# Kernel tuning notes

Hardware: AMD Instinct MI355X
Metric: run time of the kernel (lower is better)

## Reference

```python
import jax, jax.numpy as jnp
import numpy as np


def _shift(w):
    # max(0, -min(w)): scalar shift making w + shift non-negative
    return jnp.maximum(0.0, -jnp.min(w))


def shifted_linear(x, W, b=None):
    # F.linear with non-negative weights plus row-sum correction
    alpha = _shift(W)
    y = x @ (W + alpha).T - alpha * jnp.sum(x, axis=-1, keepdims=True)
    if b is not None:
        y = y + b
    return y


def shifted_depthwise_conv(x, w, b):
    # x: (B, D, L), w: (D, 1, K) depthwise; causal-style padding K-1, sliced to L by caller
    alpha = _shift(w)
    k = w.shape[2]
    pad = k - 1
    dn = ('NCH', 'OIH', 'NCH')
    groups = w.shape[0]
    y = jax.lax.conv_general_dilated(x, w + alpha, (1,), [(pad, pad)],
                                     dimension_numbers=dn, feature_group_count=groups)
    ones_k = jnp.ones_like(w)
    ssum = jax.lax.conv_general_dilated(x, ones_k, (1,), [(pad, pad)],
                                        dimension_numbers=dn, feature_group_count=groups)
    return y - alpha * ssum + b[None, :, None]


def setup_inputs() -> dict:
    key = jax.random.key(0)
    ks = jax.random.split(key, 10)
    d_model, d_inner, d_state, d_conv, dt_rank = 1024, 2048, 16, 4, 64
    B, L = 2, 1024
    s = 0.05
    return {
        'hidden_states': jax.random.normal(ks[0], (B, L, d_model), jnp.float32),
        'W_in': jax.random.normal(ks[1], (2 * d_inner, d_model), jnp.float32) * s,
        'conv_w': jax.random.normal(ks[2], (d_inner, 1, d_conv), jnp.float32) * 0.3,
        'conv_b': jax.random.normal(ks[3], (d_inner,), jnp.float32) * s,
        'W_x': jax.random.normal(ks[4], (dt_rank + 2 * d_state, d_inner), jnp.float32) * s,
        'W_dt': jax.random.normal(ks[5], (d_inner, dt_rank), jnp.float32) * s,
        'dt_bias': jax.random.normal(ks[6], (d_inner,), jnp.float32),
        'W_out': jax.random.normal(ks[7], (d_model, d_inner), jnp.float32) * s,
        'A_log': jax.random.normal(ks[8], (d_inner, d_state), jnp.float32) * 0.5,
        'D': jax.random.normal(ks[9], (d_inner,), jnp.float32),
    }


def reference(hidden_states, W_in, conv_w, conv_b, W_x, W_dt, dt_bias, W_out, A_log, D):
    b, l, dm = hidden_states.shape
    d_inner = conv_w.shape[0]
    d_state = A_log.shape[1]
    dt_rank = W_dt.shape[1]

    A = jnp.exp(A_log)  # (d_inner, d_state), always positive

    # in_proj over (b*l, d_model) -> (b, 2*d_inner, l)
    xz = shifted_linear(hidden_states.reshape(b * l, dm), W_in)
    xz = xz.reshape(b, l, 2 * d_inner).transpose(0, 2, 1)
    x, z = xz[:, :d_inner], xz[:, d_inner:]

    # depthwise shifted conv + SiLU activation, truncated to seqlen
    x = jax.nn.silu(shifted_depthwise_conv(x, conv_w, conv_b)[..., :l])

    # x_proj -> dt_raw, B, C
    x_dbl = shifted_linear(x.transpose(0, 2, 1).reshape(b * l, d_inner), W_x)
    dt_raw = x_dbl[:, :dt_rank]
    Bm = x_dbl[:, dt_rank:dt_rank + d_state].reshape(b, l, d_state).transpose(0, 2, 1)  # (b,n,l)
    Cm = x_dbl[:, dt_rank + d_state:].reshape(b, l, d_state).transpose(0, 2, 1)         # (b,n,l)
    dt = shifted_linear(dt_raw, W_dt).reshape(b, l, d_inner).transpose(0, 2, 1)          # (b,d,l)

    # delta activation (softplus) with bias, clamped
    delta = jnp.clip(jax.nn.softplus(dt + dt_bias[None, :, None]), 1e-4, 20.0)

    # global scalar shifts for B and C
    beta = _shift(Bm)
    gamma = _shift(Cm)
    B_nn = Bm + beta
    C_nn = Cm + gamma

    # precomputed per-step operands, scan axis first: (l, b, d, n)
    deltaA = jnp.exp(-jnp.einsum('bdl,dn->lbdn', delta, A))
    dBu = jnp.einsum('bdl,bnl,bdl->lbdn', delta, B_nn, x)
    C_scan = C_nn.transpose(2, 0, 1)  # (l, b, n)

    def step(xc, inp):
        dA_i, dBu_i, C_i = inp
        xc = dA_i * xc + dBu_i                                   # (b,d,n)
        y = jnp.einsum('bdn,bn->bd', xc, C_i) - gamma * jnp.sum(xc, axis=-1)
        return xc, y

    x0 = jnp.zeros((b, d_inner, d_state), dtype=delta.dtype)
    _, ys = jax.lax.scan(step, x0, (deltaA, dBu, C_scan))        # ys: (l, b, d)

    y = ys.transpose(1, 2, 0) + x * D[None, :, None]             # (b, d, l) skip term
    y = y * jax.nn.silu(z)                                       # gate activation

    out = shifted_linear(y.transpose(0, 2, 1).reshape(b * l, d_inner), W_out)
    return out.reshape(b, l, dm)
```

## Files before the change

### kernel.cpp

```cpp
#include <hip/hip_runtime.h>
#include <hip/hip_bf16.h>
#include <math.h>

#define DM 1024
#define DI 2048
#define DS 16
#define DTR 64
#define NB 2
#define LL 1024
#define TT (NB*LL)
#define SCH 16
#define NCH (LL/SCH)

typedef unsigned short u16;
typedef __attribute__((ext_vector_type(8))) short bf16x8;
typedef __attribute__((ext_vector_type(4))) float f32x4;

#define LOG2E 1.4426950408889634f

__device__ inline u16 f2bf(float f) {
  union { float f; unsigned u; } c; c.f = f;
  unsigned u = c.u;
  return (u16)((u + 0x7fffu + ((u >> 16) & 1u)) >> 16);
}

#define GLDS16(g, l) __builtin_amdgcn_global_load_lds( \
    (const __attribute__((address_space(1))) unsigned int*)(g), \
    (__attribute__((address_space(3))) unsigned int*)(l), 16, 0, 0)

template<int BM, int BN, int EPI>
__global__ __launch_bounds__(256) void gemm_bf16(
    const u16* __restrict__ A, const u16* __restrict__ B,
    float* __restrict__ C, int M, int N, int K, int kpb,
    const float* __restrict__ bias) {
  constexpr int WAVES_M = BM / 64;
  constexpr int WAVES_N = 4 / WAVES_M;
  constexpr int WTM = 4;
  constexpr int WTN = BN / (WAVES_N * 16);
  constexpr int ASLABS = BM / 16;
  constexpr int SLABS = (BM + BN) / 16;
  constexpr int SPW = SLABS / 4;
  __shared__ u16 As[BM * 32];
  __shared__ u16 Bs[BN * 32];
  const int tid = threadIdx.x;
  const int wave = tid >> 6;
  const int lane = tid & 63;
  const int bm = blockIdx.y * BM;
  const int bn = blockIdx.x * BN;
  const int wm = (wave / WAVES_N) * 64;
  const int wn = (wave % WAVES_N) * (WTN * 16);
  const int r4 = lane >> 2;
  const int kc = (lane & 3) * 8;
  const int fr = lane & 15;
  const int fq = lane >> 4;
  const int koff = blockIdx.z * kpb;
  C += (size_t)blockIdx.z * M * N;

  f32x4 acc[WTM][WTN];
#pragma unroll
  for (int i = 0; i < WTM; ++i)
#pragma unroll
    for (int j = 0; j < WTN; ++j) acc[i][j] = (f32x4){0.f, 0.f, 0.f, 0.f};

  for (int k0 = koff; k0 < koff + kpb; k0 += 32) {
#pragma unroll
    for (int s = wave * SPW; s < (wave + 1) * SPW; ++s) {
      if (s < ASLABS) {
        int row = s * 16 + r4;
        GLDS16(A + (size_t)(bm + row) * K + k0 + kc, &As[s * 512]);
      } else {
        int row = (s - ASLABS) * 16 + r4;
        GLDS16(B + (size_t)(bn + row) * K + k0 + kc, &Bs[(s - ASLABS) * 512]);
      }
    }
    __syncthreads();
    bf16x8 af[WTM], bf[WTN];
#pragma unroll
    for (int i = 0; i < WTM; ++i)
      af[i] = *(const bf16x8*)&As[(wm + 16 * i + fr) * 32 + fq * 8];
#pragma unroll
    for (int j = 0; j < WTN; ++j)
      bf[j] = *(const bf16x8*)&Bs[(wn + 16 * j + fr) * 32 + fq * 8];
#pragma unroll
    for (int i = 0; i < WTM; ++i)
#pragma unroll
      for (int j = 0; j < WTN; ++j)
        acc[i][j] = __builtin_amdgcn_mfma_f32_16x16x32_bf16(af[i], bf[j], acc[i][j], 0, 0, 0);
    __syncthreads();
  }

#pragma unroll
  for (int i = 0; i < WTM; ++i) {
    int row0 = bm + wm + 16 * i + fq * 4;
#pragma unroll
    for (int j = 0; j < WTN; ++j) {
      int col = bn + wn + 16 * j + fr;
#pragma unroll
      for (int r = 0; r < 4; ++r) {
        float v = acc[i][j][r];
        if (EPI == 1) {
          v += bias[col];
          float sp = (v > 20.0f) ? v : log1pf(expf(v));
          v = fminf(fmaxf(sp, 1e-4f), 20.0f);
        }
        C[(size_t)(row0 + r) * N + col] = v;
      }
    }
  }
}

__global__ __launch_bounds__(256) void gemm3_reduce(
    const float* __restrict__ part, float* __restrict__ xdb,
    u16* __restrict__ dtraw_bf) {
  int i = blockIdx.x * 256 + threadIdx.x;
  int t = i >> 7, col = i & 127;
  float s = 0.f;
#pragma unroll
  for (int z = 0; z < 16; ++z) s += part[(size_t)z * TT * 128 + i];
  if (col < 96) xdb[t * 96 + col] = s;
  if (col < 64) dtraw_bf[t * 64 + col] = f2bf(s);
}

__global__ __launch_bounds__(256) void cast_all(
    const float* __restrict__ hs, const float* __restrict__ win,
    const float* __restrict__ wout, const float* __restrict__ wx,
    const float* __restrict__ wdt,
    u16* __restrict__ hs_bf, u16* __restrict__ win_bf,
    u16* __restrict__ wout_bf, u16* __restrict__ wx_bf,
    u16* __restrict__ wdt_bf) {
  int gid = blockIdx.x * 256 + threadIdx.x;
  const float* src; u16* dst; int off;
  if (gid < 524288)       { src = hs;   dst = hs_bf;   off = gid; }
  else if (gid < 1572864) { src = win;  dst = win_bf;  off = gid - 524288; }
  else if (gid < 2097152) { src = wout; dst = wout_bf; off = gid - 1572864; }
  else if (gid < 2146304) { src = wx;   dst = wx_bf;   off = gid - 2097152; }
  else if (gid < 2179072) { src = wdt;  dst = wdt_bf;  off = gid - 2146304; }
  else {
    ushort4 z4 = {0, 0, 0, 0};
    ((ushort4*)wx_bf)[49152 + gid - 2179072] = z4;
    return;
  }
  float4 v = ((const float4*)src)[off];
  ushort4 o;
  o.x = f2bf(v.x); o.y = f2bf(v.y); o.z = f2bf(v.z); o.w = f2bf(v.w);
  ((ushort4*)dst)[off] = o;
}

__global__ __launch_bounds__(256) void conv_silu4(
    const float* __restrict__ xz, const float* __restrict__ w,
    const float* __restrict__ cb, float* __restrict__ xc,
    u16* __restrict__ xc_bf) {
  int gid = blockIdx.x * 256 + threadIdx.x;
  int dq = (gid & 511) * 4;
  int t = gid >> 9;
  int l = t & (LL - 1);
  float wv[4][4];
#pragma unroll
  for (int j = 0; j < 4; ++j) {
    float4 ww = *(const float4*)&w[(dq + j) * 4];
    wv[j][0] = ww.x; wv[j][1] = ww.y; wv[j][2] = ww.z; wv[j][3] = ww.w;
  }
  float4 acc = *(const float4*)&cb[dq];
#pragma unroll
  for (int k = 0; k < 4; ++k) {
    int ll = l - 3 + k;
    if (ll < 0) continue;
    float4 xv = *(const float4*)&xz[(size_t)(t - 3 + k) * (2 * DI) + dq];
    acc.x += xv.x * wv[0][k]; acc.y += xv.y * wv[1][k];
    acc.z += xv.z * wv[2][k]; acc.w += xv.w * wv[3][k];
  }
  acc.x /= (1.0f + expf(-acc.x)); acc.y /= (1.0f + expf(-acc.y));
  acc.z /= (1.0f + expf(-acc.z)); acc.w /= (1.0f + expf(-acc.w));
  *(float4*)&xc[(size_t)t * DI + dq] = acc;
  ushort4 o;
  o.x = f2bf(acc.x); o.y = f2bf(acc.y); o.z = f2bf(acc.z); o.w = f2bf(acc.w);
  *(ushort4*)&xc_bf[(size_t)t * DI + dq] = o;
}

__global__ __launch_bounds__(256) void beta_part(
    const float* __restrict__ xdb, float* __restrict__ pmin) {
  float mn = 3.4e38f;
  for (int i = blockIdx.x * 256 + threadIdx.x; i < TT * DS; i += 64 * 256) {
    int t = i >> 4, n = i & 15;
    mn = fminf(mn, xdb[t * 96 + 64 + n]);
  }
#pragma unroll
  for (int o = 32; o; o >>= 1) mn = fminf(mn, __shfl_down(mn, o));
  __shared__ float sm[4];
  if ((threadIdx.x & 63) == 0) sm[threadIdx.x >> 6] = mn;
  __syncthreads();
  if (threadIdx.x == 0)
    pmin[blockIdx.x] = fminf(fminf(sm[0], sm[1]), fminf(sm[2], sm[3]));
}

__global__ void beta_fin(const float* __restrict__ pmin, float* __restrict__ beta) {
  float mn = pmin[threadIdx.x];
#pragma unroll
  for (int o = 32; o; o >>= 1) mn = fminf(mn, __shfl_down(mn, o));
  if (threadIdx.x == 0) beta[0] = fmaxf(0.0f, -mn);
}

__global__ __launch_bounds__(256) void scan_pass1(
    const float* __restrict__ delta, const float* __restrict__ xc,
    const float* __restrict__ xdb, const float* __restrict__ A_log,
    const float* __restrict__ beta_p,
    float* __restrict__ hend, float* __restrict__ Ssum) {
  const int d = blockIdx.x * 256 + threadIdx.x;
  const int c = blockIdx.y;
  const int b = blockIdx.z;
  __shared__ float Bsh[SCH][16];
  const float beta = beta_p[0];
  const int t0 = b * LL + c * SCH;
  {
    int i = threadIdx.x;
    int tt = i >> 4, n = i & 15;
    Bsh[tt][n] = xdb[(size_t)(t0 + tt) * 96 + 64 + n] + beta;
  }
  __syncthreads();
  float Av2[16];
#pragma unroll
  for (int n = 0; n < 16; ++n) Av2[n] = expf(A_log[d * 16 + n]) * LOG2E;
  float h[16];
#pragma unroll
  for (int n = 0; n < 16; ++n) h[n] = 0.f;
  float S = 0.f;
  for (int tt = 0; tt < SCH; ++tt) {
    int t = t0 + tt;
    float dv = delta[(size_t)t * DI + d];
    float xv = xc[(size_t)t * DI + d];
    float dx = dv * xv;
    S += dv;
#pragma unroll
    for (int n = 0; n < 16; ++n) {
      float a = __builtin_amdgcn_exp2f(-dv * Av2[n]);
      h[n] = a * h[n] + dx * Bsh[tt][n];
    }
  }
  size_t base = (((size_t)(b * NCH + c) * DI) + d) * 16;
#pragma unroll
  for (int n = 0; n < 16; ++n) hend[base + n] = h[n];
  Ssum[((size_t)(b * NCH + c) * DI) + d] = S;
}

__global__ __launch_bounds__(256) void scan_pass2(
    float* __restrict__ hend, const float* __restrict__ Ssum,
    const float* __restrict__ A_log) {
  int gid = blockIdx.x * 256 + threadIdx.x;
  int n = gid & 15;
  int d = (gid >> 4) & (DI - 1);
  int b = gid >> 15;
  float Av2 = expf(A_log[d * 16 + n]) * LOG2E;
  float H = 0.f;
  for (int c = 0; c < NCH; ++c) {
    size_t cb = ((size_t)(b * NCH + c) * DI) + d;
    float hl = hend[cb * 16 + n];
    float p = __builtin_amdgcn_exp2f(-Av2 * Ssum[cb]);
    hend[cb * 16 + n] = H;
    H = p * H + hl;
  }
}

__global__ __launch_bounds__(256) void scan_pass3(
    const float* __restrict__ delta, const float* __restrict__ xc,
    const float* __restrict__ xdb, const float* __restrict__ xz,
    const float* __restrict__ A_log, const float* __restrict__ Dp,
    const float* __restrict__ beta_p, const float* __restrict__ hstart,
    u16* __restrict__ ybf) {
  const int d = blockIdx.x * 256 + threadIdx.x;
  const int c = blockIdx.y;
  const int b = blockIdx.z;
  __shared__ float Bsh[SCH][16];
  __shared__ float Csh[SCH][16];
  const float beta = beta_p[0];
  const int t0 = b * LL + c * SCH;
  {
    int i = threadIdx.x;
    int tt = i >> 4, n = i & 15;
    size_t row = (size_t)(t0 + tt) * 96;
    Bsh[tt][n] = xdb[row + 64 + n] + beta;
    Csh[tt][n] = xdb[row + 80 + n];
  }
  __syncthreads();
  float Av2[16];
#pragma unroll
  for (int n = 0; n < 16; ++n) Av2[n] = expf(A_log[d * 16 + n]) * LOG2E;
  float h[16];
  size_t base = (((size_t)(b * NCH + c) * DI) + d) * 16;
#pragma unroll
  for (int n = 0; n < 16; ++n) h[n] = hstart[base + n];
  const float Dd = Dp[d];
  for (int tt = 0; tt < SCH; ++tt) {
    int t = t0 + tt;
    float dv = delta[(size_t)t * DI + d];
    float xv = xc[(size_t)t * DI + d];
    float dx = dv * xv;
    float yv = 0.f;
#pragma unroll
    for (int n = 0; n < 16; ++n) {
      float a = __builtin_amdgcn_exp2f(-dv * Av2[n]);
      h[n] = a * h[n] + dx * Bsh[tt][n];
      yv += h[n] * Csh[tt][n];
    }
    float zv = xz[(size_t)t * (2 * DI) + DI + d];
    float out = (yv + xv * Dd) * (zv / (1.0f + expf(-zv)));
    ybf[(size_t)t * DI + d] = f2bf(out);
  }
}

extern "C" void kernel_launch(void* const* d_in, const int* in_sizes, int n_in,
                              void* d_out, int out_size, void* d_ws, size_t ws_size,
                              hipStream_t stream) {
  const float* hs      = (const float*)d_in[0];
  const float* W_in    = (const float*)d_in[1];
  const float* conv_w  = (const float*)d_in[2];
  const float* conv_b  = (const float*)d_in[3];
  const float* W_x     = (const float*)d_in[4];
  const float* W_dt    = (const float*)d_in[5];
  const float* dt_bias = (const float*)d_in[6];
  const float* W_out   = (const float*)d_in[7];
  const float* A_log   = (const float*)d_in[8];
  const float* Dp      = (const float*)d_in[9];
  float* out = (float*)d_out;

  float* ws     = (float*)d_ws;
  float* xz     = ws;
  float* xcv    = xz   + (size_t)TT * 2 * DI;
  float* xdb    = xcv  + (size_t)TT * DI;
  float* dlt    = xdb  + (size_t)TT * 96;
  float* betab  = dlt  + (size_t)TT * DI;
  float* pmin   = betab + 64;
  float* hend   = pmin + 64;
  float* Ssum   = hend + (size_t)NB * NCH * DI * 16;
  float* hs_bfR = Ssum + (size_t)NB * NCH * DI;
  float* win_bfR  = hs_bfR + (size_t)TT * DM / 2;
  float* wout_bfR = win_bfR + (size_t)2 * DI * DM / 2;
  float* xcv_bfR  = wout_bfR + (size_t)DM * DI / 2;
  float* wx_bfR   = xcv_bfR + (size_t)TT * DI / 2;
  float* wdt_bfR  = wx_bfR + 131072;
  float* dtraw_bfR = wdt_bfR + 65536;

  u16* hs_bf    = (u16*)hs_bfR;
  u16* win_bf   = (u16*)win_bfR;
  u16* wout_bf  = (u16*)wout_bfR;
  u16* xcv_bf   = (u16*)xcv_bfR;
  u16* wx_bf    = (u16*)wx_bfR;
  u16* wdt_bf   = (u16*)wdt_bfR;
  u16* dtraw_bf = (u16*)dtraw_bfR;
  u16* ybf      = (u16*)win_bfR;
  float* part   = dlt;

  dim3 blk(256);

  cast_all<<<8576, blk, 0, stream>>>(hs, W_in, W_out, W_x, W_dt,
                                     hs_bf, win_bf, wout_bf, wx_bf, wdt_bf);

  gemm_bf16<128, 128, 0><<<dim3(4096 / 128, TT / 128), blk, 0, stream>>>(
      hs_bf, win_bf, xz, TT, 2 * DI, DM, DM, nullptr);

  conv_silu4<<<(TT * DI / 4) / 256, blk, 0, stream>>>(xz, conv_w, conv_b, xcv, xcv_bf);

  gemm_bf16<128, 128, 0><<<dim3(1, TT / 128, 16), blk, 0, stream>>>(
      xcv_bf, wx_bf, part, TT, 128, DI, 128, nullptr);
  gemm3_reduce<<<(TT * 128) / 256, blk, 0, stream>>>(part, xdb, dtraw_bf);

  beta_part<<<64, blk, 0, stream>>>(xdb, pmin);
  beta_fin<<<1, 64, 0, stream>>>(pmin, betab);

  gemm_bf16<128, 128, 1><<<dim3(DI / 128, TT / 128), blk, 0, stream>>>(
      dtraw_bf, wdt_bf, dlt, TT, DI, DTR, DTR, dt_bias);

  scan_pass1<<<dim3(DI / 256, NCH, NB), blk, 0, stream>>>(
      dlt, xcv, xdb, A_log, betab, hend, Ssum);
  scan_pass2<<<(NB * DI * DS) / 256, blk, 0, stream>>>(hend, Ssum, A_log);
  scan_pass3<<<dim3(DI / 256, NCH, NB), blk, 0, stream>>>(
      dlt, xcv, xdb, xz, A_log, Dp, betab, hend, ybf);

  gemm_bf16<64, 128, 0><<<dim3(DM / 128, TT / 64), blk, 0, stream>>>(
      ybf, wout_bf, out, TT, DM, DI, DI, nullptr);
}
```

Baseline: 277.9 us.

## Store xz and conv output as bf16 and fuse beta min into reduce

The in-projection GEMM now writes xz as bf16 instead of fp32. Conv and the scan passes read bf16 xz and the bf16 conv output, and the fp32 copy of the conv output is dropped. The min reduction for the B shift now runs inside gemm3_reduce, which removes one kernel launch and one re-read of xdb. This halves activation traffic through several stages, at the cost of bf16 rounding on the x and z activations used in the scan and gate.

```diff
diff --git a/kernel.cpp b/kernel.cpp
--- a/kernel.cpp
+++ b/kernel.cpp
@@ -23,15 +23,19 @@
   unsigned u = c.u;
   return (u16)((u + 0x7fffu + ((u >> 16) & 1u)) >> 16);
 }
+__device__ inline float bf2f(u16 u) {
+  union { unsigned u; float f; } c; c.u = ((unsigned)u) << 16;
+  return c.f;
+}
 
 #define GLDS16(g, l) __builtin_amdgcn_global_load_lds( \
     (const __attribute__((address_space(1))) unsigned int*)(g), \
     (__attribute__((address_space(3))) unsigned int*)(l), 16, 0, 0)
 
-template<int BM, int BN, int EPI>
+template<int BM, int BN, int EPI, int OB>
 __global__ __launch_bounds__(256) void gemm_bf16(
     const u16* __restrict__ A, const u16* __restrict__ B,
-    float* __restrict__ C, int M, int N, int K, int kpb,
+    void* __restrict__ Cv, int M, int N, int K, int kpb,
     const float* __restrict__ bias) {
   constexpr int WAVES_M = BM / 64;
   constexpr int WAVES_N = 4 / WAVES_M;
@@ -54,7 +58,8 @@
   const int fr = lane & 15;
   const int fq = lane >> 4;
   const int koff = blockIdx.z * kpb;
-  C += (size_t)blockIdx.z * M * N;
+  float* C = (float*)Cv + (size_t)blockIdx.z * M * N;
+  u16* C16 = (u16*)Cv;
 
   f32x4 acc[WTM][WTN];
 #pragma unroll
@@ -103,7 +108,8 @@
           float sp = (v > 20.0f) ? v : log1pf(expf(v));
           v = fminf(fmaxf(sp, 1e-4f), 20.0f);
         }
-        C[(size_t)(row0 + r) * N + col] = v;
+        if (OB == 1) C16[(size_t)(row0 + r) * N + col] = f2bf(v);
+        else         C[(size_t)(row0 + r) * N + col] = v;
       }
     }
   }
@@ -111,7 +117,7 @@
 
 __global__ __launch_bounds__(256) void gemm3_reduce(
     const float* __restrict__ part, float* __restrict__ xdb,
-    u16* __restrict__ dtraw_bf) {
+    u16* __restrict__ dtraw_bf, float* __restrict__ pmin) {
   int i = blockIdx.x * 256 + threadIdx.x;
   int t = i >> 7, col = i & 127;
   float s = 0.f;
@@ -119,6 +125,28 @@
   for (int z = 0; z < 16; ++z) s += part[(size_t)z * TT * 128 + i];
   if (col < 96) xdb[t * 96 + col] = s;
   if (col < 64) dtraw_bf[t * 64 + col] = f2bf(s);
+  float mn = (col >= 64 && col < 80) ? s : 3.4e38f;
+#pragma unroll
+  for (int o = 32; o; o >>= 1) mn = fminf(mn, __shfl_down(mn, o));
+  __shared__ float sm[4];
+  if ((threadIdx.x & 63) == 0) sm[threadIdx.x >> 6] = mn;
+  __syncthreads();
+  if (threadIdx.x == 0)
+    pmin[blockIdx.x] = fminf(fminf(sm[0], sm[1]), fminf(sm[2], sm[3]));
+}
+
+__global__ __launch_bounds__(256) void beta_fin(
+    const float* __restrict__ pmin, float* __restrict__ beta) {
+  float mn = 3.4e38f;
+#pragma unroll
+  for (int k = 0; k < 4; ++k) mn = fminf(mn, pmin[threadIdx.x + 256 * k]);
+#pragma unroll
+  for (int o = 32; o; o >>= 1) mn = fminf(mn, __shfl_down(mn, o));
+  __shared__ float sm[4];
+  if ((threadIdx.x & 63) == 0) sm[threadIdx.x >> 6] = mn;
+  __syncthreads();
+  if (threadIdx.x == 0)
+    beta[0] = fmaxf(0.0f, -fminf(fminf(sm[0], sm[1]), fminf(sm[2], sm[3])));
 }
 
 __global__ __launch_bounds__(256) void cast_all(
@@ -147,9 +175,8 @@
 }
 
 __global__ __launch_bounds__(256) void conv_silu4(
-    const float* __restrict__ xz, const float* __restrict__ w,
-    const float* __restrict__ cb, float* __restrict__ xc,
-    u16* __restrict__ xc_bf) {
+    const u16* __restrict__ xz, const float* __restrict__ w,
+    const float* __restrict__ cb, u16* __restrict__ xc_bf) {
   int gid = blockIdx.x * 256 + threadIdx.x;
   int dq = (gid & 511) * 4;
   int t = gid >> 9;
@@ -165,43 +192,19 @@
   for (int k = 0; k < 4; ++k) {
     int ll = l - 3 + k;
     if (ll < 0) continue;
-    float4 xv = *(const float4*)&xz[(size_t)(t - 3 + k) * (2 * DI) + dq];
-    acc.x += xv.x * wv[0][k]; acc.y += xv.y * wv[1][k];
-    acc.z += xv.z * wv[2][k]; acc.w += xv.w * wv[3][k];
+    ushort4 xv = *(const ushort4*)&xz[(size_t)(t - 3 + k) * (2 * DI) + dq];
+    acc.x += bf2f(xv.x) * wv[0][k]; acc.y += bf2f(xv.y) * wv[1][k];
+    acc.z += bf2f(xv.z) * wv[2][k]; acc.w += bf2f(xv.w) * wv[3][k];
   }
   acc.x /= (1.0f + expf(-acc.x)); acc.y /= (1.0f + expf(-acc.y));
   acc.z /= (1.0f + expf(-acc.z)); acc.w /= (1.0f + expf(-acc.w));
-  *(float4*)&xc[(size_t)t * DI + dq] = acc;
   ushort4 o;
   o.x = f2bf(acc.x); o.y = f2bf(acc.y); o.z = f2bf(acc.z); o.w = f2bf(acc.w);
   *(ushort4*)&xc_bf[(size_t)t * DI + dq] = o;
 }
 
-__global__ __launch_bounds__(256) void beta_part(
-    const float* __restrict__ xdb, float* __restrict__ pmin) {
-  float mn = 3.4e38f;
-  for (int i = blockIdx.x * 256 + threadIdx.x; i < TT * DS; i += 64 * 256) {
-    int t = i >> 4, n = i & 15;
-    mn = fminf(mn, xdb[t * 96 + 64 + n]);
-  }
-#pragma unroll
-  for (int o = 32; o; o >>= 1) mn = fminf(mn, __shfl_down(mn, o));
-  __shared__ float sm[4];
-  if ((threadIdx.x & 63) == 0) sm[threadIdx.x >> 6] = mn;
-  __syncthreads();
-  if (threadIdx.x == 0)
-    pmin[blockIdx.x] = fminf(fminf(sm[0], sm[1]), fminf(sm[2], sm[3]));
-}
-
-__global__ void beta_fin(const float* __restrict__ pmin, float* __restrict__ beta) {
-  float mn = pmin[threadIdx.x];
-#pragma unroll
-  for (int o = 32; o; o >>= 1) mn = fminf(mn, __shfl_down(mn, o));
-  if (threadIdx.x == 0) beta[0] = fmaxf(0.0f, -mn);
-}
-
 __global__ __launch_bounds__(256) void scan_pass1(
-    const float* __restrict__ delta, const float* __restrict__ xc,
+    const float* __restrict__ delta, const u16* __restrict__ xc_bf,
     const float* __restrict__ xdb, const float* __restrict__ A_log,
     const float* __restrict__ beta_p,
     float* __restrict__ hend, float* __restrict__ Ssum) {
@@ -227,7 +230,7 @@
   for (int tt = 0; tt < SCH; ++tt) {
     int t = t0 + tt;
     float dv = delta[(size_t)t * DI + d];
-    float xv = xc[(size_t)t * DI + d];
+    float xv = bf2f(xc_bf[(size_t)t * DI + d]);
     float dx = dv * xv;
     S += dv;
 #pragma unroll
@@ -261,8 +264,8 @@
 }
 
 __global__ __launch_bounds__(256) void scan_pass3(
-    const float* __restrict__ delta, const float* __restrict__ xc,
-    const float* __restrict__ xdb, const float* __restrict__ xz,
+    const float* __restrict__ delta, const u16* __restrict__ xc_bf,
+    const float* __restrict__ xdb, const u16* __restrict__ xz_bf,
     const float* __restrict__ A_log, const float* __restrict__ Dp,
     const float* __restrict__ beta_p, const float* __restrict__ hstart,
     u16* __restrict__ ybf) {
@@ -292,7 +295,7 @@
   for (int tt = 0; tt < SCH; ++tt) {
     int t = t0 + tt;
     float dv = delta[(size_t)t * DI + d];
-    float xv = xc[(size_t)t * DI + d];
+    float xv = bf2f(xc_bf[(size_t)t * DI + d]);
     float dx = dv * xv;
     float yv = 0.f;
 #pragma unroll
@@ -301,7 +304,7 @@
       h[n] = a * h[n] + dx * Bsh[tt][n];
       yv += h[n] * Csh[tt][n];
     }
-    float zv = xz[(size_t)t * (2 * DI) + DI + d];
+    float zv = bf2f(xz_bf[(size_t)t * (2 * DI) + DI + d]);
     float out = (yv + xv * Dd) * (zv / (1.0f + expf(-zv)));
     ybf[(size_t)t * DI + d] = f2bf(out);
   }
@@ -322,27 +325,27 @@
   const float* Dp      = (const float*)d_in[9];
   float* out = (float*)d_out;
 
-  float* ws     = (float*)d_ws;
-  float* xz     = ws;
-  float* xcv    = xz   + (size_t)TT * 2 * DI;
-  float* xdb    = xcv  + (size_t)TT * DI;
-  float* dlt    = xdb  + (size_t)TT * 96;
-  float* betab  = dlt  + (size_t)TT * DI;
-  float* pmin   = betab + 64;
-  float* hend   = pmin + 64;
-  float* Ssum   = hend + (size_t)NB * NCH * DI * 16;
-  float* hs_bfR = Ssum + (size_t)NB * NCH * DI;
-  float* win_bfR  = hs_bfR + (size_t)TT * DM / 2;
+  float* ws      = (float*)d_ws;
+  float* xz_bfR  = ws;
+  float* xcv_bfR = xz_bfR + (size_t)TT * 2 * DI / 2;
+  float* xdb     = xcv_bfR + (size_t)TT * DI / 2;
+  float* dlt     = xdb + (size_t)TT * 96;
+  float* betab   = dlt + (size_t)TT * DI;
+  float* pmin    = betab + 64;
+  float* hend    = pmin + 1024;
+  float* Ssum    = hend + (size_t)NB * NCH * DI * 16;
+  float* hs_bfR  = Ssum + (size_t)NB * NCH * DI;
+  float* win_bfR = hs_bfR + (size_t)TT * DM / 2;
   float* wout_bfR = win_bfR + (size_t)2 * DI * DM / 2;
-  float* xcv_bfR  = wout_bfR + (size_t)DM * DI / 2;
-  float* wx_bfR   = xcv_bfR + (size_t)TT * DI / 2;
-  float* wdt_bfR  = wx_bfR + 131072;
+  float* wx_bfR  = wout_bfR + (size_t)DM * DI / 2;
+  float* wdt_bfR = wx_bfR + 131072;
   float* dtraw_bfR = wdt_bfR + 65536;
 
+  u16* xz_bf    = (u16*)xz_bfR;
+  u16* xcv_bf   = (u16*)xcv_bfR;
   u16* hs_bf    = (u16*)hs_bfR;
   u16* win_bf   = (u16*)win_bfR;
   u16* wout_bf  = (u16*)wout_bfR;
-  u16* xcv_bf   = (u16*)xcv_bfR;
   u16* wx_bf    = (u16*)wx_bfR;
   u16* wdt_bf   = (u16*)wdt_bfR;
   u16* dtraw_bf = (u16*)dtraw_bfR;
@@ -354,27 +357,26 @@
   cast_all<<<8576, blk, 0, stream>>>(hs, W_in, W_out, W_x, W_dt,
                                      hs_bf, win_bf, wout_bf, wx_bf, wdt_bf);
 
-  gemm_bf16<128, 128, 0><<<dim3(4096 / 128, TT / 128), blk, 0, stream>>>(
-      hs_bf, win_bf, xz, TT, 2 * DI, DM, DM, nullptr);
-
-  conv_silu4<<<(TT * DI / 4) / 256, blk, 0, stream>>>(xz, conv_w, conv_b, xcv, xcv_bf);
-
-  gemm_bf16<128, 128, 0><<<dim3(1, TT / 128, 16), blk, 0, stream>>>(
+  gemm_bf16<128, 128, 0, 1><<<dim3(4096 / 128, TT / 128), blk, 0, stream>>>(
+      hs_bf, win_bf, xz_bf, TT, 2 * DI, DM, DM, nullptr);
+
+  conv_silu4<<<(TT * DI / 4) / 256, blk, 0, stream>>>(xz_bf, conv_w, conv_b, xcv_bf);
+
+  gemm_bf16<128, 128, 0, 0><<<dim3(1, TT / 128, 16), blk, 0, stream>>>(
       xcv_bf, wx_bf, part, TT, 128, DI, 128, nullptr);
-  gemm3_reduce<<<(TT * 128) / 256, blk, 0, stream>>>(part, xdb, dtraw_bf);
-
-  beta_part<<<64, blk, 0, stream>>>(xdb, pmin);
-  beta_fin<<<1, 64, 0, stream>>>(pmin, betab);
-
-  gemm_bf16<128, 128, 1><<<dim3(DI / 128, TT / 128), blk, 0, stream>>>(
+  gemm3_reduce<<<(TT * 128) / 256, blk, 0, stream>>>(part, xdb, dtraw_bf, pmin);
+
+  beta_fin<<<1, blk, 0, stream>>>(pmin, betab);
+
+  gemm_bf16<128, 128, 1, 0><<<dim3(DI / 128, TT / 128), blk, 0, stream>>>(
       dtraw_bf, wdt_bf, dlt, TT, DI, DTR, DTR, dt_bias);
 
   scan_pass1<<<dim3(DI / 256, NCH, NB), blk, 0, stream>>>(
-      dlt, xcv, xdb, A_log, betab, hend, Ssum);
+      dlt, xcv_bf, xdb, A_log, betab, hend, Ssum);
   scan_pass2<<<(NB * DI * DS) / 256, blk, 0, stream>>>(hend, Ssum, A_log);
   scan_pass3<<<dim3(DI / 256, NCH, NB), blk, 0, stream>>>(
-      dlt, xcv, xdb, xz, A_log, Dp, betab, hend, ybf);
-
-  gemm_bf16<64, 128, 0><<<dim3(DM / 128, TT / 64), blk, 0, stream>>>(
+      dlt, xcv_bf, xdb, xz_bf, A_log, Dp, betab, hend, ybf);
+
+  gemm_bf16<64, 128, 0, 0><<<dim3(DM / 128, TT / 64), blk, 0, stream>>>(
       ybf, wout_bf, out, TT, DM, DI, DI, nullptr);
 }
```

New measurement: 271.4 us. 1.02x faster.
